# Kernel optimization log

Hardware: AMD Instinct MI355X
Metric: run time of the kernel (lower is better)

Reference implementation:

```python
import jax, jax.numpy as jnp
import numpy as np

ALPHA = 0.0
EPSILON = 1e-4
STD = 1.0


def _T_arr(h, std):
    # T(linspace(-10,10,h), std) from the torch module
    x = jnp.linspace(-10.0, 10.0, h)
    dx = (x[-1] - x[0]) / (h - 1)
    dispx = (h % 2 - 1) / 2.0
    g = -jnp.exp(-((x - dx * dispx) ** 2) / (2.0 * std ** 2))  # -gaussian(a=1)
    g = g + jnp.max(jnp.abs(g))
    return g / jnp.max(jnp.abs(g))


def setup_inputs() -> dict:
    key = jax.random.key(0)
    k1, k2 = jax.random.split(key)
    B, H = 512, 256
    return {
        "recon": jax.random.normal(k1, (B, H), dtype=jnp.float32),
        "target": jax.random.normal(k2, (B, H), dtype=jnp.float32),
    }


def reference(recon, target):
    B, h = recon.shape
    # Batched Toeplitz: D[b, i, j] = target[b, i-j] if 0 <= i-j < h else 0
    rows = jnp.arange(2 * h - 1)[:, None]
    cols = jnp.arange(h)[None, :]
    idx = rows - cols                                  # (2h-1, h)
    valid = (idx >= 0) & (idx < h)
    D = jnp.where(valid, target[:, jnp.clip(idx, 0, h - 1)], 0.0)  # [B, 2h-1, h]

    # Normal matrix + diagonal regularization: v = DtD + diag(alpha*diag(DtD) + eps)
    DtD = jnp.einsum('bij,bik->bjk', D, D)             # [B, h, h]
    dia = jnp.diagonal(DtD, axis1=1, axis2=2)          # [B, h]
    ar = jnp.arange(h)
    A = DtD.at[:, ar, ar].add(ALPHA * dia + EPSILON)

    # pad recon to length 2h-1 (centered, left = floor((h-1)/2))
    pad_l = (h - 1) // 2
    pad_r = (h - 1) - pad_l
    rp = jnp.pad(recon, ((0, 0), (pad_l, pad_r)))      # [B, 2h-1]
    b = jnp.einsum('bij,bi->bj', D, rp)                # D^T @ padded recon

    v = jnp.linalg.solve(A, b[..., None])[..., 0]      # [B, h] matched filters

    T = _T_arr(h, STD)
    num = jnp.sqrt(jnp.sum((T[None, :] * v) ** 2, axis=1))
    den = jnp.sqrt(jnp.sum(v ** 2, axis=1))
    return jnp.sum(0.5 * num / den)                    # reduction='sum'
```

## Files before the change

kernel.cpp:

```cpp
#include <hip/hip_runtime.h>
#include <math.h>

#define H 256
#define EPS 1e-4f

template <int CTRL>
__device__ __forceinline__ float dpp0(float x) {
    return __int_as_float(
        __builtin_amdgcn_update_dpp(0, __float_as_int(x), CTRL, 0xf, 0xf, true));
}
__device__ __forceinline__ float rdlane(float x, int l) {
    return __int_as_float(__builtin_amdgcn_readlane(__float_as_int(x), l));
}
__device__ __forceinline__ float frcp_fast(float v) { return __builtin_amdgcn_rcpf(v); }
__device__ __forceinline__ float frcp_nr(float v) {
    float r = __builtin_amdgcn_rcpf(v);
    return fmaf(r, fmaf(-v, r, 1.0f), r);
}
__device__ __forceinline__ void wave_red_sum2(float& a, float& b) {
    a += dpp0<0x111>(a);  b += dpp0<0x111>(b);
    a += dpp0<0x112>(a);  b += dpp0<0x112>(b);
    a += dpp0<0x114>(a);  b += dpp0<0x114>(b);
    a += dpp0<0x118>(a);  b += dpp0<0x118>(b);
    a += dpp0<0x142>(a);  b += dpp0<0x142>(b);
    a += dpp0<0x143>(a);  b += dpp0<0x143>(b);
    a = rdlane(a, 63);
    b = rdlane(b, 63);
}

#define STEP(KF1, KF2, LN1, LN2) do {                                   \
    float g  = -sF * isB;                                               \
    float sE = fmaf(g, sF, sB);                       \
    isB = frcp_fast(sE);                                                \
    float mu = sR * isB;                                                \
    float rlF2 = rdlane(F[KF2], (LN2));                   \
    float rlB1 = rdlane(Bv[KF1], (LN1));                  \
    float rlR2 = rdlane(Rv[KF2], (LN2));                  \
    sF = fmaf(g, rlB1, rlF2);                         \
    float tB2 = fmaf(g, rlF2, rlB1);                  \
    sR = fmaf(-mu, tB2, rlR2);                        \
    sB = sE;                                                            \
    float sb0 = dpp0<0x138>(Bv[3]);                     \
    float sr0 = dpp0<0x138>(rav[3]);                                    \
    float nB0 = fmaf(g, F[0], sb0);                                     \
    float nB1 = fmaf(g, F[1], Bv[0]);                                   \
    float nB2 = fmaf(g, F[2], Bv[1]);                                   \
    float nB3 = fmaf(g, F[3], Bv[2]);                                   \
    float nF0 = fmaf(g, sb0,  F[0]);                                    \
    float nF1 = fmaf(g, Bv[0], F[1]);                                   \
    float nF2 = fmaf(g, Bv[1], F[2]);                                   \
    float nF3 = fmaf(g, Bv[2], F[3]);                                   \
    float nr0 = fmaf(g, av[0], sr0);                                    \
    float nr1 = fmaf(g, av[1], rav[0]);                                 \
    float nr2 = fmaf(g, av[2], rav[1]);                                 \
    float nr3 = fmaf(g, av[3], rav[2]);                                 \
    float na0 = fmaf(g, sr0,   av[0]);                                  \
    float na1 = fmaf(g, rav[0], av[1]);                                 \
    float na2 = fmaf(g, rav[1], av[2]);                                 \
    float na3 = fmaf(g, rav[2], av[3]);                                 \
    xv[0] = fmaf(mu, nr0, xv[0]);  Rv[0] = fmaf(-mu, nB0, Rv[0]);       \
    xv[1] = fmaf(mu, nr1, xv[1]);  Rv[1] = fmaf(-mu, nB1, Rv[1]);       \
    xv[2] = fmaf(mu, nr2, xv[2]);  Rv[2] = fmaf(-mu, nB2, Rv[2]);       \
    xv[3] = fmaf(mu, nr3, xv[3]);  Rv[3] = fmaf(-mu, nB3, Rv[3]);       \
    Bv[0]=nB0; Bv[1]=nB1; Bv[2]=nB2; Bv[3]=nB3;                         \
    F[0]=nF0; F[1]=nF1; F[2]=nF2; F[3]=nF3;                             \
    av[0]=na0; av[1]=na1; av[2]=na2; av[3]=na3;                         \
    rav[0]=nr0; rav[1]=nr1; rav[2]=nr2; rav[3]=nr3;                     \
} while (0)

__global__ __launch_bounds__(64) void awloss_batch(
        const float* __restrict__ recon,
        const float* __restrict__ target,
        float* __restrict__ losses) {
    const int b    = blockIdx.x;
    const int lane = threadIdx.x;
    const bool l0  = (lane == 0);

    __shared__ __align__(16) float tgtp[576];
    __shared__ __align__(16) float recp[576];

    const float4 tv4 = ((const float4*)(target + b * H))[lane];
    const float4 rv4 = ((const float4*)(recon  + b * H))[lane];

    #pragma unroll
    for (int c = 0; c < 9; ++c) { tgtp[c*64+lane] = 0.f; recp[c*64+lane] = 0.f; }
    __syncthreads();
    *(float4*)&tgtp[4*lane] = tv4;
    recp[127 + 4*lane + 0] = rv4.x;
    recp[127 + 4*lane + 1] = rv4.y;
    recp[127 + 4*lane + 2] = rv4.z;
    recp[127 + 4*lane + 3] = rv4.w;
    __syncthreads();

    float racc[4] = {0.f,0.f,0.f,0.f}, bacc[4] = {0.f,0.f,0.f,0.f};
    float4 W0t = *(const float4*)&tgtp[4*lane];
    float4 W0r = *(const float4*)&recp[4*lane];
    for (int m0 = 0; m0 < 256; m0 += 4) {
        float4 W1t = *(const float4*)&tgtp[m0 + 4 + 4*lane];
        float4 W1r = *(const float4*)&recp[m0 + 4 + 4*lane];
        float t0s = rdlane(W0t.x, 0);
        float t1s = rdlane(W0t.y, 0);
        float t2s = rdlane(W0t.z, 0);
        float t3s = rdlane(W0t.w, 0);
        racc[0] = fmaf(t0s, W0t.x, racc[0]); bacc[0] = fmaf(t0s, W0r.x, bacc[0]);
        racc[1] = fmaf(t0s, W0t.y, racc[1]); bacc[1] = fmaf(t0s, W0r.y, bacc[1]);
        racc[2] = fmaf(t0s, W0t.z, racc[2]); bacc[2] = fmaf(t0s, W0r.z, bacc[2]);
        racc[3] = fmaf(t0s, W0t.w, racc[3]); bacc[3] = fmaf(t0s, W0r.w, bacc[3]);
        racc[0] = fmaf(t1s, W0t.y, racc[0]); bacc[0] = fmaf(t1s, W0r.y, bacc[0]);
        racc[1] = fmaf(t1s, W0t.z, racc[1]); bacc[1] = fmaf(t1s, W0r.z, bacc[1]);
        racc[2] = fmaf(t1s, W0t.w, racc[2]); bacc[2] = fmaf(t1s, W0r.w, bacc[2]);
        racc[3] = fmaf(t1s, W1t.x, racc[3]); bacc[3] = fmaf(t1s, W1r.x, bacc[3]);
        racc[0] = fmaf(t2s, W0t.z, racc[0]); bacc[0] = fmaf(t2s, W0r.z, bacc[0]);
        racc[1] = fmaf(t2s, W0t.w, racc[1]); bacc[1] = fmaf(t2s, W0r.w, bacc[1]);
        racc[2] = fmaf(t2s, W1t.x, racc[2]); bacc[2] = fmaf(t2s, W1r.x, bacc[2]);
        racc[3] = fmaf(t2s, W1t.y, racc[3]); bacc[3] = fmaf(t2s, W1r.y, bacc[3]);
        racc[0] = fmaf(t3s, W0t.w, racc[0]); bacc[0] = fmaf(t3s, W0r.w, bacc[0]);
        racc[1] = fmaf(t3s, W1t.x, racc[1]); bacc[1] = fmaf(t3s, W1r.x, bacc[1]);
        racc[2] = fmaf(t3s, W1t.y, racc[2]); bacc[2] = fmaf(t3s, W1r.y, bacc[2]);
        racc[3] = fmaf(t3s, W1t.z, racc[3]); bacc[3] = fmaf(t3s, W1r.z, bacc[3]);
        W0t = W1t; W0r = W1r;
    }

    float t0v = rdlane(racc[0], 0) + EPS;
    float it0 = frcp_nr(t0v);
    float F[4], Bv[4], av[4], rav[4], xv[4], Rv[4];
    #pragma unroll
    for (int c = 0; c < 4; ++c) {
        float rh = racc[c] * it0;
        if (c == 0) rh = l0 ? 1.0f : rh;
        F[c] = rh; Bv[c] = rh;
    }
    float bb0 = rdlane(bacc[0], 0) * it0;
    #pragma unroll
    for (int c = 0; c < 4; ++c) {
        float bvv = bacc[c] * it0;
        Rv[c] = fmaf(-bb0, F[c], bvv);
        xv[c] = 0.f; av[c] = 0.f; rav[c] = 0.f;
    }
    if (l0) { xv[0] = bb0; av[0] = 1.0f; rav[0] = 1.0f; }

    float sF  = rdlane(F[1], 0);
    float sB  = 1.0f, isB = 1.0f;
    float sR  = rdlane(Rv[1], 0);

    #pragma unroll
    for (int t = 0; t < 63; ++t) {
        STEP(1, 2, t, t);
        STEP(2, 3, t, t);
        STEP(3, 0, t, t + 1);
        STEP(0, 1, t + 1, t + 1);
    }
    STEP(1, 2, 63, 63);
    STEP(2, 3, 63, 63);
    {
        float g  = -sF * isB;
        float sE = fmaf(g, sF, sB);
        float mu = sR * frcp_fast(sE);
        float sr0 = dpp0<0x138>(rav[3]);
        xv[0] = fmaf(mu, fmaf(g, av[0], sr0),    xv[0]);
        xv[1] = fmaf(mu, fmaf(g, av[1], rav[0]), xv[1]);
        xv[2] = fmaf(mu, fmaf(g, av[2], rav[1]), xv[2]);
        xv[3] = fmaf(mu, fmaf(g, av[3], rav[2]), xv[3]);
    }

    float sT = 0.f, sV = 0.f;
    const float dxg = 20.0f / 255.0f;
    #pragma unroll
    for (int c = 0; c < 4; ++c) {
        float v  = xv[c];
        float u  = -10.0f + dxg * (float)(4*lane + c) + 0.5f * dxg;
        float Ti = 1.0f - expf(-0.5f * u * u);
        float tw = Ti * v;
        sT += tw * tw;
        sV += v * v;
    }
    wave_red_sum2(sT, sV);
    if (l0) losses[b] = 0.5f * sqrtf(sT / sV);
}

__global__ __launch_bounds__(64) void awloss_reduce(
        const float* __restrict__ losses, float* __restrict__ out) {
    int lane = threadIdx.x;
    float s = 0.f;
    #pragma unroll
    for (int c = 0; c < 8; ++c) s += losses[c * 64 + lane];
    float d = 0.f;
    wave_red_sum2(s, d);
    if (lane == 0) out[0] = s;
}

extern "C" void kernel_launch(void* const* d_in, const int* in_sizes, int n_in,
                              void* d_out, int out_size, void* d_ws, size_t ws_size,
                              hipStream_t stream) {
    const float* recon  = (const float*)d_in[0];
    const float* target = (const float*)d_in[1];
    float* losses = (float*)d_ws;
    float* out    = (float*)d_out;

    awloss_batch<<<512, 64, 0, stream>>>(recon, target, losses);
    awloss_reduce<<<1, 64, 0, stream>>>(losses, out);
}
```

Before: 30.95 us.

## Merge solution and residual vectors into in-place Levinson-Schur recurrence

Restructures the per-step Toeplitz solver recurrence so the solution is stored in place inside the residual vector. This removes the separate xv, av and rav arrays and roughly halves the per-lane FMAs per step, with a lane-select writing the new coefficient each step. The outer step loop is also no longer fully unrolled, trading code size for loop overhead. The serial scalar chain of reciprocal and readlane per step is unchanged, and the rearranged recurrence may change numerical behaviour.

```diff
diff --git a/kernel.cpp b/kernel.cpp
--- a/kernel.cpp
+++ b/kernel.cpp
@@ -32,40 +32,32 @@
     float g  = -sF * isB;                                               \
     float sE = fmaf(g, sF, sB);                       \
     isB = frcp_fast(sE);                                                \
-    float mu = sR * isB;                                                \
-    float rlF2 = rdlane(F[KF2], (LN2));                   \
-    float rlB1 = rdlane(Bv[KF1], (LN1));                  \
-    float rlR2 = rdlane(Rv[KF2], (LN2));                  \
-    sF = fmaf(g, rlB1, rlF2);                         \
+    float mu = -sRt * isB;                                              \
+    float rlF2 = rdlane(P[KF2], (LN2));                  \
+    float rlB1 = rdlane(Q[KF1], (LN1));                  \
+    float rlR2 = rdlane(X[KF2], (LN2));                  \
+    sF  = fmaf(g, rlB1, rlF2);                        \
     float tB2 = fmaf(g, rlF2, rlB1);                  \
-    sR = fmaf(-mu, tB2, rlR2);                        \
-    sB = sE;                                                            \
-    float sb0 = dpp0<0x138>(Bv[3]);                     \
-    float sr0 = dpp0<0x138>(rav[3]);                                    \
-    float nB0 = fmaf(g, F[0], sb0);                                     \
-    float nB1 = fmaf(g, F[1], Bv[0]);                                   \
-    float nB2 = fmaf(g, F[2], Bv[1]);                                   \
-    float nB3 = fmaf(g, F[3], Bv[2]);                                   \
-    float nF0 = fmaf(g, sb0,  F[0]);                                    \
-    float nF1 = fmaf(g, Bv[0], F[1]);                                   \
-    float nF2 = fmaf(g, Bv[1], F[2]);                                   \
-    float nF3 = fmaf(g, Bv[2], F[3]);                                   \
-    float nr0 = fmaf(g, av[0], sr0);                                    \
-    float nr1 = fmaf(g, av[1], rav[0]);                                 \
-    float nr2 = fmaf(g, av[2], rav[1]);                                 \
-    float nr3 = fmaf(g, av[3], rav[2]);                                 \
-    float na0 = fmaf(g, sr0,   av[0]);                                  \
-    float na1 = fmaf(g, rav[0], av[1]);                                 \
-    float na2 = fmaf(g, rav[1], av[2]);                                 \
-    float na3 = fmaf(g, rav[2], av[3]);                                 \
-    xv[0] = fmaf(mu, nr0, xv[0]);  Rv[0] = fmaf(-mu, nB0, Rv[0]);       \
-    xv[1] = fmaf(mu, nr1, xv[1]);  Rv[1] = fmaf(-mu, nB1, Rv[1]);       \
-    xv[2] = fmaf(mu, nr2, xv[2]);  Rv[2] = fmaf(-mu, nB2, Rv[2]);       \
-    xv[3] = fmaf(mu, nr3, xv[3]);  Rv[3] = fmaf(-mu, nB3, Rv[3]);       \
-    Bv[0]=nB0; Bv[1]=nB1; Bv[2]=nB2; Bv[3]=nB3;                         \
-    F[0]=nF0; F[1]=nF1; F[2]=nF2; F[3]=nF3;                             \
-    av[0]=na0; av[1]=na1; av[2]=na2; av[3]=na3;                         \
-    rav[0]=nr0; rav[1]=nr1; rav[2]=nr2; rav[3]=nr3;                     \
+    sRt = fmaf(mu, tB2, rlR2);                       \
+    sB  = sE;                                                           \
+    float shq0 = dpp0<0x138>(Q[3]);                     \
+    float nQ0 = fmaf(g, P[0], shq0);                                    \
+    float nQ1 = fmaf(g, P[1], Q[0]);                                    \
+    float nQ2 = fmaf(g, P[2], Q[1]);                                    \
+    float nQ3 = fmaf(g, P[3], Q[2]);                                    \
+    float nP0 = fmaf(g, shq0, P[0]);                                    \
+    float nP1 = fmaf(g, Q[0],  P[1]);                                   \
+    float nP2 = fmaf(g, Q[1],  P[2]);                                   \
+    float nP3 = fmaf(g, Q[2],  P[3]);                                   \
+    X[0] = fmaf(mu, nQ0, X[0]);                                         \
+    X[1] = fmaf(mu, nQ1, X[1]);                                         \
+    X[2] = fmaf(mu, nQ2, X[2]);                                         \
+    X[3] = fmaf(mu, nQ3, X[3]);                                         \
+    bool bm = (lane == (LN1));                  \
+    P[0]=nP0; P[1]=nP1; P[2]=nP2; P[3]=nP3;                             \
+    Q[0]=nQ0; Q[1]=nQ1; Q[2]=nQ2; Q[3]=nQ3;                             \
+    P[KF1] = bm ? g  : P[KF1];                                          \
+    X[KF1] = bm ? mu : X[KF1];                                          \
 } while (0)
 
 __global__ __launch_bounds__(64) void awloss_batch(
@@ -123,27 +115,25 @@
 
     float t0v = rdlane(racc[0], 0) + EPS;
     float it0 = frcp_nr(t0v);
-    float F[4], Bv[4], av[4], rav[4], xv[4], Rv[4];
+    float P[4], Q[4], X[4];
     #pragma unroll
     for (int c = 0; c < 4; ++c) {
         float rh = racc[c] * it0;
         if (c == 0) rh = l0 ? 1.0f : rh;
-        F[c] = rh; Bv[c] = rh;
+        P[c] = rh; Q[c] = rh;
     }
     float bb0 = rdlane(bacc[0], 0) * it0;
     #pragma unroll
     for (int c = 0; c < 4; ++c) {
         float bvv = bacc[c] * it0;
-        Rv[c] = fmaf(-bb0, F[c], bvv);
-        xv[c] = 0.f; av[c] = 0.f; rav[c] = 0.f;
+        X[c] = fmaf(bb0, P[c], -bvv);
     }
-    if (l0) { xv[0] = bb0; av[0] = 1.0f; rav[0] = 1.0f; }
+    if (l0) X[0] = bb0;
 
-    float sF  = rdlane(F[1], 0);
+    float sF  = rdlane(P[1], 0);
     float sB  = 1.0f, isB = 1.0f;
-    float sR  = rdlane(Rv[1], 0);
+    float sRt = rdlane(X[1], 0);
 
-    #pragma unroll
     for (int t = 0; t < 63; ++t) {
         STEP(1, 2, t, t);
         STEP(2, 3, t, t);
@@ -155,19 +145,24 @@
     {
         float g  = -sF * isB;
         float sE = fmaf(g, sF, sB);
-        float mu = sR * frcp_fast(sE);
-        float sr0 = dpp0<0x138>(rav[3]);
-        xv[0] = fmaf(mu, fmaf(g, av[0], sr0),    xv[0]);
-        xv[1] = fmaf(mu, fmaf(g, av[1], rav[0]), xv[1]);
-        xv[2] = fmaf(mu, fmaf(g, av[2], rav[1]), xv[2]);
-        xv[3] = fmaf(mu, fmaf(g, av[3], rav[2]), xv[3]);
+        float mu = -sRt * frcp_fast(sE);
+        float shq0 = dpp0<0x138>(Q[3]);
+        float nQ0 = fmaf(g, P[0], shq0);
+        float nQ1 = fmaf(g, P[1], Q[0]);
+        float nQ2 = fmaf(g, P[2], Q[1]);
+        float nQ3 = fmaf(g, P[3], Q[2]);
+        X[0] = fmaf(mu, nQ0, X[0]);
+        X[1] = fmaf(mu, nQ1, X[1]);
+        X[2] = fmaf(mu, nQ2, X[2]);
+        X[3] = fmaf(mu, nQ3, X[3]);
+        X[3] = (lane == 63) ? mu : X[3];
     }
 
     float sT = 0.f, sV = 0.f;
     const float dxg = 20.0f / 255.0f;
     #pragma unroll
     for (int c = 0; c < 4; ++c) {
-        float v  = xv[c];
+        float v  = X[c];
         float u  = -10.0f + dxg * (float)(4*lane + c) + 0.5f * dxg;
         float Ti = 1.0f - expf(-0.5f * u * u);
         float tw = Ti * v;
```

After: 27.24 us. 12.0% less time.
